# Kernel optimization log

Hardware: AMD Instinct MI355X
Metric: run time of the kernel (lower is better)

The kernel has to match this reference:

```python
import jax, jax.numpy as jnp
import numpy as np

N, E, D, H, G, O = 50000, 800000, 128, 256, 128, 10
BN_EPS = 1e-5
SLOPE = 0.2  # LeakyReLU negative slope


def setup_inputs() -> dict:
    keys = iter(jax.random.split(jax.random.key(0), 64))

    def rn(shape, scale=0.05):
        return jax.random.normal(next(keys), shape, jnp.float32) * scale

    inp = {
        "x": jax.random.normal(next(keys), (N, D), jnp.float32),
        "edge_index": jax.random.randint(next(keys), (2, E), 0, N),
        "edge_attr": jax.random.normal(next(keys), (E, 3), jnp.float32),
        "batch": jnp.sort(jax.random.randint(next(keys), (N,), 0, G)),
    }
    for i, din in zip((1, 2, 3), (D, H, H)):
        inp[f"We{i}"] = rn((3, din))
        inp[f"be{i}"] = jnp.zeros((din,), jnp.float32)
        inp[f"W{i}1"] = rn((din, H))
        inp[f"b{i}1"] = jnp.zeros((H,), jnp.float32)
        inp[f"g{i}"] = jnp.ones((H,), jnp.float32)
        inp[f"bt{i}"] = jnp.zeros((H,), jnp.float32)
        inp[f"mu{i}"] = jnp.zeros((H,), jnp.float32)
        inp[f"var{i}"] = jnp.ones((H,), jnp.float32)
        inp[f"W{i}2"] = rn((H, H))
        inp[f"b{i}2"] = jnp.zeros((H,), jnp.float32)
    for name, shape in (("Wm1", (3 * H, 200)), ("Wm2", (200, 200)), ("Wm3", (200, 200)), ("Wm4", (200, O))):
        inp[name] = rn(shape)
        inp["b" + name[1:]] = jnp.zeros((shape[1],), jnp.float32)
    return inp


def _leaky(v):
    return jax.nn.leaky_relu(v, SLOPE)


def _gine(x, src, dst, ea, We, be, W1, b1, g, bt, mu, var, W2, b2):
    # message: ReLU(x_j + lin_edge(edge_attr)); aggregate: scatter-sum to dst
    msg = jax.nn.relu(x[src] + ea @ We + be)          # [E, din]
    agg = jax.ops.segment_sum(msg, dst, num_segments=N)  # [N, din]
    h = x + agg                                       # (1+eps)*x_i + agg, eps=0
    h = h @ W1 + b1
    h = g * (h - mu) * jax.lax.rsqrt(var + BN_EPS) + bt  # BatchNorm1d (eval)
    h = _leaky(h)
    return _leaky(h @ W2 + b2)


def reference(x, edge_index, edge_attr, batch,
              We1, be1, W11, b11, g1, bt1, mu1, var1, W12, b12,
              We2, be2, W21, b21, g2, bt2, mu2, var2, W22, b22,
              We3, be3, W31, b31, g3, bt3, mu3, var3, W32, b32,
              Wm1, bm1, Wm2, bm2, Wm3, bm3, Wm4, bm4):
    src, dst = edge_index[0], edge_index[1]
    x1 = _gine(x, src, dst, edge_attr, We1, be1, W11, b11, g1, bt1, mu1, var1, W12, b12)
    x2 = _gine(x1, src, dst, edge_attr, We2, be2, W21, b21, g2, bt2, mu2, var2, W22, b22)
    x3 = _gine(x2, src, dst, edge_attr, We3, be3, W31, b31, g3, bt3, mu3, var3, W32, b32)
    p1 = jax.ops.segment_sum(x1, batch, num_segments=G)  # global_add_pool
    p2 = jax.ops.segment_sum(x2, batch, num_segments=G)
    p3 = jax.ops.segment_sum(x3, batch, num_segments=G)
    h = jnp.concatenate((p1, p2, p3), axis=1)            # [G, 3H]
    # MLP (dropout is identity at inference); note doubled LeakyReLU in source
    h = _leaky(_leaky(h @ Wm1 + bm1))
    h = _leaky(_leaky(h @ Wm2 + bm2))
    h = _leaky(_leaky(h @ Wm3 + bm3))
    return h @ Wm4 + bm4                                 # [G, O]
```

## Files before the change

### kernel.cpp

```cpp
#include <hip/hip_runtime.h>
#include <hip/hip_fp16.h>

#define LRELU(v) ((v) >= 0.f ? (v) : 0.2f * (v))
#define DLRELU(v) ((v) >= 0.f ? (v) : 0.04f * (v))

constexpr int Nn = 50000;
constexpr int Ee = 800000;
constexpr int Hh = 256;
constexpr int Gg = 128;
constexpr int Oo = 10;

typedef __attribute__((ext_vector_type(8))) short short8;
typedef __attribute__((ext_vector_type(4))) float f32x4;
typedef __attribute__((ext_vector_type(4))) unsigned int uv4;
typedef __attribute__((ext_vector_type(2))) unsigned int uv2;
typedef __attribute__((ext_vector_type(4))) unsigned short us4;

__device__ inline unsigned short f2h(float f) {
  __half h = __float2half_rn(f);
  return *reinterpret_cast<unsigned short*>(&h);
}
__device__ inline float h2f(unsigned short u) {
  __half h = *reinterpret_cast<__half*>(&u);
  return __half2float(h);
}
__device__ inline __half2 u2h2(unsigned int u) {
  return *reinterpret_cast<__half2*>(&u);
}
__device__ inline unsigned int h22u(__half2 h) {
  return *reinterpret_cast<unsigned int*>(&h);
}
__device__ inline __half2 hmax2(__half2 a, __half2 b) {
  __half2 r;
  asm volatile("v_pk_max_f16 %0, %1, %2" : "=v"(r) : "v"(a), "v"(b));
  return r;
}
__device__ inline unsigned short f2bf(float f) {
  union { float f; unsigned int i; } v; v.f = f;
  unsigned int i = v.i;
  return (unsigned short)((i + 0x7FFFu + ((i >> 16) & 1u)) >> 16);
}

typedef __attribute__((address_space(1))) const unsigned int gu32;
typedef __attribute__((address_space(3))) unsigned int lu32;
__device__ inline void gload_lds16(const void* g, void* l) {
  __builtin_amdgcn_global_load_lds((gu32*)g, (lu32*)l, 16, 0, 0);
}

__global__ __launch_bounds__(256) void hist_kernel(
    const int* __restrict__ dst, int* __restrict__ deg)
{
  const int e = blockIdx.x * 256 + threadIdx.x;
  if (e < Ee) atomicAdd(&deg[dst[e]], 1);
}

__global__ __launch_bounds__(1024) void scan1_kernel(
    const int* __restrict__ deg, int* __restrict__ bsum)
{
  const int i = blockIdx.x * 1024 + threadIdx.x;
  int v = (i < Nn) ? deg[i] : 0;
  #pragma unroll
  for (int o = 32; o; o >>= 1) v += __shfl_xor(v, o, 64);
  __shared__ int ws[16];
  const int wid = threadIdx.x >> 6, lane = threadIdx.x & 63;
  if (lane == 0) ws[wid] = v;
  __syncthreads();
  if (threadIdx.x == 0) {
    int s = 0;
    #pragma unroll
    for (int k = 0; k < 16; k++) s += ws[k];
    bsum[blockIdx.x] = s;
  }
}

__global__ __launch_bounds__(64) void scan2_kernel(
    const int* __restrict__ bsum, int* __restrict__ boff, int* __restrict__ row_ptr, int nb)
{
  if (threadIdx.x == 0) {
    int s = 0;
    for (int b = 0; b < nb; b++) { boff[b] = s; s += bsum[b]; }
    row_ptr[Nn] = s;
  }
}

__global__ __launch_bounds__(1024) void scan3_kernel(
    const int* __restrict__ deg, const int* __restrict__ boff,
    int* __restrict__ row_ptr, int* __restrict__ cursor)
{
  const int i = blockIdx.x * 1024 + threadIdx.x;
  const int wid = threadIdx.x >> 6, lane = threadIdx.x & 63;
  const int v = (i < Nn) ? deg[i] : 0;
  int inc = v;
  #pragma unroll
  for (int o = 1; o < 64; o <<= 1) {
    const int u = __shfl_up(inc, o, 64);
    if (lane >= o) inc += u;
  }
  __shared__ int ws[16];
  if (lane == 63) ws[wid] = inc;
  __syncthreads();
  if (wid == 0 && lane < 16) {
    int s = ws[lane];
    #pragma unroll
    for (int o = 1; o < 16; o <<= 1) {
      const int u = __shfl_up(s, o, 64);
      if (lane >= o) s += u;
    }
    ws[lane] = s;
  }
  __syncthreads();
  const int woff = (wid == 0) ? 0 : ws[wid - 1];
  const int excl = boff[blockIdx.x] + woff + inc - v;
  if (i < Nn) { row_ptr[i] = excl; cursor[i] = excl; }
}

__global__ __launch_bounds__(256) void fill_kernel(
    const int* __restrict__ src, const int* __restrict__ dst,
    const float* __restrict__ ea, int* __restrict__ cursor,
    uv4* __restrict__ edges)
{
  const int e = blockIdx.x * 256 + threadIdx.x;
  if (e >= Ee) return;
  const int pos = atomicAdd(&cursor[dst[e]], 1);
  uv4 r;
  r.x = (unsigned)src[e];
  r.y = h22u(__float2half2_rn(ea[3 * e + 0]));
  r.z = h22u(__float2half2_rn(ea[3 * e + 1]));
  r.w = h22u(__float2half2_rn(ea[3 * e + 2]));
  edges[pos] = r;
}

__global__ __launch_bounds__(256) void f2h_kernel(
    const float* __restrict__ in, unsigned short* __restrict__ out, int n4)
{
  const int i = blockIdx.x * 256 + threadIdx.x;
  if (i >= n4) return;
  const float4 v = *reinterpret_cast<const float4*>(in + (size_t)i * 4);
  us4 o; o.x = f2h(v.x); o.y = f2h(v.y); o.z = f2h(v.z); o.w = f2h(v.w);
  *reinterpret_cast<us4*>(out + (size_t)i * 4) = o;
}

struct WtJobs {
  const float* src[10];
  unsigned short* dst[10];
  int K[10], M[10], Kpad[10], isbf[10], blk0[11];
};

__global__ __launch_bounds__(256) void wtall_kernel(WtJobs J)
{
  int j = 0;
  #pragma unroll
  for (int q = 1; q < 10; q++) if ((int)blockIdx.x >= J.blk0[q]) j = q;
  const int g = ((int)blockIdx.x - J.blk0[j]) * 256 + threadIdx.x;
  const int Kpad = J.Kpad[j];
  if (g >= 256 * Kpad) return;
  const int c = g / Kpad, k = g % Kpad;
  const int K = J.K[j], M = J.M[j];
  unsigned short o = 0;
  if (c < M && k < K) {
    const float w = J.src[j][(size_t)k * M + c];
    o = J.isbf[j] ? f2bf(w) : f2h(w);
  }
  J.dst[j][(size_t)c * Kpad + k] = o;
}

template<int DIN>
__global__ __launch_bounds__(256) void agg_gather(
    const unsigned short* __restrict__ x, const uv4* __restrict__ edges,
    const float* __restrict__ We, const float* __restrict__ be,
    const int* __restrict__ row_ptr, unsigned short* __restrict__ S)
{
  constexpr int FPL = DIN / 64;
  constexpr int H2  = FPL / 2;
  constexpr int SH  = (DIN == 256) ? 8 : 7;
  const int wv   = threadIdx.x >> 6;
  const int lane = threadIdx.x & 63;
  const int n = blockIdx.x * 4 + wv;
  if (n >= Nn) return;
  const int fo = lane * FPL;

  const __half2 zero2 = __float2half2_rn(0.f);
  __half2 w0h[H2], w1h[H2], w2h[H2], bbh[H2], acc[H2];
  #pragma unroll
  for (int j = 0; j < H2; j++) {
    w0h[j] = __halves2half2(__float2half_rn(We[0 * DIN + fo + 2 * j]),
                            __float2half_rn(We[0 * DIN + fo + 2 * j + 1]));
    w1h[j] = __halves2half2(__float2half_rn(We[1 * DIN + fo + 2 * j]),
                            __float2half_rn(We[1 * DIN + fo + 2 * j + 1]));
    w2h[j] = __halves2half2(__float2half_rn(We[2 * DIN + fo + 2 * j]),
                            __float2half_rn(We[2 * DIN + fo + 2 * j + 1]));
    bbh[j] = __halves2half2(__float2half_rn(be[fo + 2 * j]),
                            __float2half_rn(be[fo + 2 * j + 1]));
    acc[j] = zero2;
  }

  const int beg = row_ptr[n], end = row_ptr[n + 1];
  int i = beg;

  for (; i + 8 <= end; i += 8) {
    uv4 e[8];
    #pragma unroll
    for (int q = 0; q < 8; q++) e[q] = __builtin_nontemporal_load(edges + i + q);
    __half2 xv[8][H2];
    #pragma unroll
    for (int q = 0; q < 8; q++) {
      const unsigned o = (e[q].x << SH) + fo;
      if constexpr (H2 == 2) {
        const uv2 r = *reinterpret_cast<const uv2*>(x + o);
        xv[q][0] = u2h2(r.x); xv[q][1] = u2h2(r.y);
      } else {
        xv[q][0] = u2h2(*reinterpret_cast<const unsigned int*>(x + o));
      }
    }
    #pragma unroll
    for (int q = 0; q < 8; q++) {
      const __half2 a0 = u2h2(e[q].y), a1 = u2h2(e[q].z), a2 = u2h2(e[q].w);
      #pragma unroll
      for (int j = 0; j < H2; j++) {
        __half2 m = __hadd2(xv[q][j], bbh[j]);
        m = __hfma2(a2, w2h[j], m);
        m = __hfma2(a1, w1h[j], m);
        m = __hfma2(a0, w0h[j], m);
        acc[j] = __hadd2(acc[j], hmax2(m, zero2));
      }
    }
  }
  for (; i < end; i++) {
    const uv4 e0 = __builtin_nontemporal_load(edges + i);
    const unsigned o0 = (e0.x << SH) + fo;
    __half2 xv0[H2];
    if constexpr (H2 == 2) {
      const uv2 r0 = *reinterpret_cast<const uv2*>(x + o0);
      xv0[0] = u2h2(r0.x); xv0[1] = u2h2(r0.y);
    } else {
      xv0[0] = u2h2(*reinterpret_cast<const unsigned int*>(x + o0));
    }
    const __half2 a00 = u2h2(e0.y), a01 = u2h2(e0.z), a02 = u2h2(e0.w);
    #pragma unroll
    for (int j = 0; j < H2; j++) {
      __half2 m0 = __hadd2(xv0[j], bbh[j]);
      m0 = __hfma2(a02, w2h[j], m0);
      m0 = __hfma2(a01, w1h[j], m0);
      m0 = __hfma2(a00, w0h[j], m0);
      acc[j] = __hadd2(acc[j], hmax2(m0, zero2));
    }
  }

  const unsigned on = ((unsigned)n << SH) + fo;
  if constexpr (H2 == 2) {
    const uv2 rs = *reinterpret_cast<const uv2*>(x + on);
    const float2 s0 = __half22float2(u2h2(rs.x)), s1 = __half22float2(u2h2(rs.y));
    const float2 f0 = __half22float2(acc[0]), f1 = __half22float2(acc[1]);
    uv2 o;
    o.x = (unsigned)f2h(s0.x + f0.x) | ((unsigned)f2h(s0.y + f0.y) << 16);
    o.y = (unsigned)f2h(s1.x + f1.x) | ((unsigned)f2h(s1.y + f1.y) << 16);
    __builtin_nontemporal_store(o, reinterpret_cast<uv2*>(S + on));
  } else {
    const float2 s0 = __half22float2(u2h2(*reinterpret_cast<const unsigned int*>(x + on)));
    const float2 f0 = __half22float2(acc[0]);
    const unsigned o = (unsigned)f2h(s0.x + f0.x) | ((unsigned)f2h(s0.y + f0.y) << 16);
    __builtin_nontemporal_store(o, reinterpret_cast<unsigned int*>(S + on));
  }
}

template<int K1, bool WRITE_XB>
__global__ __launch_bounds__(512) void gemm12(
    const unsigned short* __restrict__ A,
    const unsigned short* __restrict__ B1t, const float* __restrict__ b1,
    const float* __restrict__ gamma, const float* __restrict__ beta,
    const float* __restrict__ mu, const float* __restrict__ var,
    const unsigned short* __restrict__ B2t, const float* __restrict__ b2,
    unsigned short* __restrict__ XB,
    const int* __restrict__ batch, float* __restrict__ pooled, int layer)
{
  __shared__ __align__(16) unsigned short smem[128 * 256];
  unsigned short* lA = smem;
  unsigned short* lY = smem;
  float* part = (float*)smem;

  const int t = threadIdx.x;
  const int lane = t & 63, wid = t >> 6;
  const int wrow = wid >> 2, wcol = wid & 3;
  const int l15 = lane & 15, hi = lane >> 4;
  const int n0 = blockIdx.x * 128;

  constexpr int SPR = K1 / 8;
  constexpr int NCH = 128 * K1 * 2 / 1024;
  constexpr int CPW = NCH / 8;
  #pragma unroll
  for (int c = 0; c < CPW; c++) {
    const int ch = wid * CPW + c;
    const int row = ch * (512 / K1) + lane / SPR;
    const int slot = lane % SPR;
    const int scol = (slot ^ (row & 7)) * 8;
    const int gr = min(n0 + row, Nn - 1);
    gload_lds16(A + (size_t)gr * K1 + scol, (char*)lA + ch * 1024);
  }
  __syncthreads();

  f32x4 acc[4][4] = {};
  #pragma unroll
  for (int ks = 0; ks < K1 / 32; ks++) {
    short8 av[4], bv[4];
    #pragma unroll
    for (int rf = 0; rf < 4; rf++) {
      const int ar = wrow * 64 + rf * 16 + l15;
      av[rf] = *reinterpret_cast<const short8*>(
          (const char*)lA + ar * (K1 * 2) + (((ks * 4 + hi) ^ (ar & 7)) << 4));
    }
    #pragma unroll
    for (int cf = 0; cf < 4; cf++) {
      const int c = wcol * 64 + cf * 16 + l15;
      bv[cf] = *reinterpret_cast<const short8*>(B1t + (size_t)c * K1 + ks * 32 + hi * 8);
    }
    #pragma unroll
    for (int rf = 0; rf < 4; rf++)
      #pragma unroll
      for (int cf = 0; cf < 4; cf++)
        acc[rf][cf] = __builtin_amdgcn_mfma_f32_16x16x32_f16(av[rf], bv[cf], acc[rf][cf], 0, 0, 0);
  }
  __syncthreads();

  #pragma unroll
  for (int cf = 0; cf < 4; cf++) {
    const int c = wcol * 64 + cf * 16 + l15;
    const float bs = b1[c];
    const float gm = gamma[c], bt2 = beta[c], mm = mu[c];
    const float iv = rsqrtf(var[c] + 1e-5f);
    const int slot0 = c >> 3;
    #pragma unroll
    for (int rf = 0; rf < 4; rf++)
      #pragma unroll
      for (int rg = 0; rg < 4; rg++) {
        const int row = wrow * 64 + rf * 16 + hi * 4 + rg;
        float v = acc[rf][cf][rg] + bs;
        v = gm * (v - mm) * iv + bt2;
        v = LRELU(v);
        *reinterpret_cast<unsigned short*>(
            (char*)lY + row * 512 + (((slot0 ^ (row & 7)) << 4)) + (c & 7) * 2) = f2h(v);
      }
  }
  __syncthreads();

  #pragma unroll
  for (int rf = 0; rf < 4; rf++)
    #pragma unroll
    for (int cf = 0; cf < 4; cf++) acc[rf][cf] = (f32x4){0.f, 0.f, 0.f, 0.f};
  #pragma unroll
  for (int ks = 0; ks < 8; ks++) {
    short8 av[4], bv[4];
    #pragma unroll
    for (int rf = 0; rf < 4; rf++) {
      const int ar = wrow * 64 + rf * 16 + l15;
      av[rf] = *reinterpret_cast<const short8*>(
          (const char*)lY + ar * 512 + (((ks * 4 + hi) ^ (ar & 7)) << 4));
    }
    #pragma unroll
    for (int cf = 0; cf < 4; cf++) {
      const int c = wcol * 64 + cf * 16 + l15;
      bv[cf] = *reinterpret_cast<const short8*>(B2t + (size_t)c * 256 + ks * 32 + hi * 8);
    }
    #pragma unroll
    for (int rf = 0; rf < 4; rf++)
      #pragma unroll
      for (int cf = 0; cf < 4; cf++)
        acc[rf][cf] = __builtin_amdgcn_mfma_f32_16x16x32_f16(av[rf], bv[cf], acc[rf][cf], 0, 0, 0);
  }
  __syncthreads();

  for (int z = t; z < 1024; z += 512) part[z] = 0.f;
  __syncthreads();

  const int base = batch[min(n0, Nn - 1)];
  int slotArr[4][4];
  #pragma unroll
  for (int rf = 0; rf < 4; rf++)
    #pragma unroll
    for (int rg = 0; rg < 4; rg++) {
      const int row = n0 + wrow * 64 + rf * 16 + hi * 4 + rg;
      slotArr[rf][rg] = (row < Nn) ? (batch[row] - base) : -1;
    }

  #pragma unroll
  for (int cf = 0; cf < 4; cf++) {
    const int col = wcol * 64 + cf * 16 + l15;
    const float bs = b2[col];
    float psum[4] = {0.f, 0.f, 0.f, 0.f};
    #pragma unroll
    for (int rf = 0; rf < 4; rf++)
      #pragma unroll
      for (int rg = 0; rg < 4; rg++) {
        const int sl = slotArr[rf][rg];
        if (sl < 0) continue;
        const float v = LRELU(acc[rf][cf][rg] + bs);
        if (WRITE_XB) {
          const int row = n0 + wrow * 64 + rf * 16 + hi * 4 + rg;
          XB[(size_t)row * 256 + col] = f2h(v);
        }
        psum[sl] += v;
      }
    #pragma unroll
    for (int k = 0; k < 4; k++)
      if (psum[k] != 0.f) atomicAdd(&part[k * 256 + col], psum[k]);
  }
  __syncthreads();

  for (int z = t; z < 1024; z += 512) {
    const float v = part[z];
    if (v != 0.f) {
      const int g = base + (z >> 8);
      if (g < Gg)
        atomicAdd(&pooled[(size_t)g * 768 + layer * 256 + (z & 255)], v);
    }
  }
}

__global__ __launch_bounds__(256) void head_fused(
    const float* __restrict__ P,
    const unsigned short* __restrict__ B1t,
    const unsigned short* __restrict__ B2t,
    const unsigned short* __restrict__ B3t,
    const unsigned short* __restrict__ B4t,
    const float* __restrict__ b1, const float* __restrict__ b2,
    const float* __restrict__ b3, const float* __restrict__ b4,
    float* __restrict__ out)
{
  __shared__ __align__(16) unsigned short act[32 * 256];
  const int t = threadIdx.x, lane = t & 63, wid = t >> 6;
  const int l15 = lane & 15, hi = lane >> 4;
  const int r0 = blockIdx.x * 32;

  f32x4 acc[2][4];

  #pragma unroll
  for (int rf = 0; rf < 2; rf++)
    #pragma unroll
    for (int cf = 0; cf < 4; cf++) acc[rf][cf] = (f32x4){0.f, 0.f, 0.f, 0.f};
  for (int ks = 0; ks < 24; ks++) {
    short8 bv[4], av[2];
    #pragma unroll
    for (int cf = 0; cf < 4; cf++) {
      const int c = wid * 64 + cf * 16 + l15;
      bv[cf] = *reinterpret_cast<const short8*>(B1t + (size_t)c * 768 + ks * 32 + hi * 8);
    }
    #pragma unroll
    for (int rf = 0; rf < 2; rf++) {
      const float* p = P + (size_t)(r0 + rf * 16 + l15) * 768 + ks * 32 + hi * 8;
      const float4 p0 = *reinterpret_cast<const float4*>(p);
      const float4 p1 = *reinterpret_cast<const float4*>(p + 4);
      short8 a;
      a[0] = (short)f2bf(p0.x); a[1] = (short)f2bf(p0.y);
      a[2] = (short)f2bf(p0.z); a[3] = (short)f2bf(p0.w);
      a[4] = (short)f2bf(p1.x); a[5] = (short)f2bf(p1.y);
      a[6] = (short)f2bf(p1.z); a[7] = (short)f2bf(p1.w);
      av[rf] = a;
    }
    #pragma unroll
    for (int rf = 0; rf < 2; rf++)
      #pragma unroll
      for (int cf = 0; cf < 4; cf++)
        acc[rf][cf] = __builtin_amdgcn_mfma_f32_16x16x32_bf16(av[rf], bv[cf], acc[rf][cf], 0, 0, 0);
  }
  #pragma unroll
  for (int cf = 0; cf < 4; cf++) {
    const int c = wid * 64 + cf * 16 + l15;
    const float bs = (c < 200) ? b1[c] : 0.f;
    const int slot0 = c >> 3;
    #pragma unroll
    for (int rf = 0; rf < 2; rf++)
      #pragma unroll
      for (int rg = 0; rg < 4; rg++) {
        const int row = rf * 16 + hi * 4 + rg;
        const float v = DLRELU(acc[rf][cf][rg] + bs);
        act[row * 256 + ((slot0 ^ (row & 7)) << 3) + (c & 7)] = f2bf(v);
      }
  }
  __syncthreads();

  #pragma unroll
  for (int L = 0; L < 2; L++) {
    const unsigned short* B = (L == 0) ? B2t : B3t;
    const float* bias = (L == 0) ? b2 : b3;
    #pragma unroll
    for (int rf = 0; rf < 2; rf++)
      #pragma unroll
      for (int cf = 0; cf < 4; cf++) acc[rf][cf] = (f32x4){0.f, 0.f, 0.f, 0.f};
    #pragma unroll
    for (int ks = 0; ks < 8; ks++) {
      short8 bv[4], av[2];
      #pragma unroll
      for (int cf = 0; cf < 4; cf++) {
        const int c = wid * 64 + cf * 16 + l15;
        bv[cf] = *reinterpret_cast<const short8*>(B + (size_t)c * 256 + ks * 32 + hi * 8);
      }
      #pragma unroll
      for (int rf = 0; rf < 2; rf++) {
        const int row = rf * 16 + l15;
        const int slot = ks * 4 + hi;
        av[rf] = *reinterpret_cast<const short8*>(
            act + row * 256 + ((slot ^ (row & 7)) << 3));
      }
      #pragma unroll
      for (int rf = 0; rf < 2; rf++)
        #pragma unroll
        for (int cf = 0; cf < 4; cf++)
          acc[rf][cf] = __builtin_amdgcn_mfma_f32_16x16x32_bf16(av[rf], bv[cf], acc[rf][cf], 0, 0, 0);
    }
    __syncthreads();
    #pragma unroll
    for (int cf = 0; cf < 4; cf++) {
      const int c = wid * 64 + cf * 16 + l15;
      const float bs = (c < 200) ? bias[c] : 0.f;
      const int slot0 = c >> 3;
      #pragma unroll
      for (int rf = 0; rf < 2; rf++)
        #pragma unroll
        for (int rg = 0; rg < 4; rg++) {
          const int row = rf * 16 + hi * 4 + rg;
          const float v = DLRELU(acc[rf][cf][rg] + bs);
          act[row * 256 + ((slot0 ^ (row & 7)) << 3) + (c & 7)] = f2bf(v);
        }
    }
    __syncthreads();
  }

  if (wid == 0) {
    f32x4 a4[2] = {};
    #pragma unroll
    for (int ks = 0; ks < 8; ks++) {
      short8 av[2];
      const short8 bv = *reinterpret_cast<const short8*>(
          B4t + (size_t)l15 * 256 + ks * 32 + hi * 8);
      #pragma unroll
      for (int rf = 0; rf < 2; rf++) {
        const int row = rf * 16 + l15;
        const int slot = ks * 4 + hi;
        av[rf] = *reinterpret_cast<const short8*>(
            act + row * 256 + ((slot ^ (row & 7)) << 3));
      }
      #pragma unroll
      for (int rf = 0; rf < 2; rf++)
        a4[rf] = __builtin_amdgcn_mfma_f32_16x16x32_bf16(av[rf], bv, a4[rf], 0, 0, 0);
    }
    if (l15 < Oo) {
      const float bs = b4[l15];
      #pragma unroll
      for (int rf = 0; rf < 2; rf++)
        #pragma unroll
        for (int rg = 0; rg < 4; rg++) {
          const int row = r0 + rf * 16 + hi * 4 + rg;
          out[(size_t)row * Oo + l15] = a4[rf][rg] + bs;
        }
    }
  }
}

extern "C" void kernel_launch(void* const* d_in, const int* in_sizes, int n_in,
                              void* d_out, int out_size, void* d_ws, size_t ws_size,
                              hipStream_t stream)
{
  const float* x     = (const float*)d_in[0];
  const int*   ei    = (const int*)d_in[1];
  const float* ea    = (const float*)d_in[2];
  const int*   batch = (const int*)d_in[3];
  const int* src = ei;
  const int* dst = ei + Ee;

  const float *We[3], *be_[3], *W1[3], *b1[3], *g_[3], *bt_[3], *mu_[3], *var_[3], *W2[3], *b2[3];
  for (int l = 0; l < 3; l++) {
    const int base = 4 + l * 10;
    We[l]  = (const float*)d_in[base + 0];
    be_[l] = (const float*)d_in[base + 1];
    W1[l]  = (const float*)d_in[base + 2];
    b1[l]  = (const float*)d_in[base + 3];
    g_[l]  = (const float*)d_in[base + 4];
    bt_[l] = (const float*)d_in[base + 5];
    mu_[l] = (const float*)d_in[base + 6];
    var_[l]= (const float*)d_in[base + 7];
    W2[l]  = (const float*)d_in[base + 8];
    b2[l]  = (const float*)d_in[base + 9];
  }
  const float *Wm[4], *bm[4];
  for (int i = 0; i < 4; i++) {
    Wm[i] = (const float*)d_in[34 + 2 * i];
    bm[i] = (const float*)d_in[35 + 2 * i];
  }

  int* deg     = (int*)d_ws;
  int* cursor  = deg + Nn;
  int* row_ptr = cursor + Nn;
  int* bsum    = row_ptr + Nn + 4;
  int* boff    = bsum + 64;
  uv4* edges   = (uv4*)(boff + 64);
  unsigned short* x0h  = (unsigned short*)(edges + Ee);
  unsigned short* Wt11 = x0h + (size_t)Nn * 128;
  unsigned short* Wt12 = Wt11 + 32768;
  unsigned short* Wt21 = Wt12 + 65536;
  unsigned short* Wt22 = Wt21 + 65536;
  unsigned short* Wt31 = Wt22 + 65536;
  unsigned short* Wt32 = Wt31 + 65536;
  unsigned short* HW1t = Wt32 + 65536;
  unsigned short* HW2t = HW1t + 256 * 768;
  unsigned short* HW3t = HW2t + 65536;
  unsigned short* HW4t = HW3t + 65536;
  unsigned short* S    = HW4t + 65536;
  unsigned short* XB0  = S  + (size_t)Nn * Hh;
  unsigned short* XB1  = XB0 + (size_t)Nn * Hh;
  float* pooled = (float*)(XB1 + (size_t)Nn * Hh);
  float* outf  = (float*)d_out;

  const int  gemmGrid = (Nn + 127) / 128;
  const int  aggGrid  = (Nn + 3) / 4;
  const int  eGrid    = (Ee + 255) / 256;
  const int  sGrid    = (Nn + 1023) / 1024;

  hipMemsetAsync(deg, 0, Nn * sizeof(int), stream);
  hipMemsetAsync(pooled, 0, (size_t)Gg * 768 * sizeof(float), stream);

  hist_kernel<<<eGrid, 256, 0, stream>>>(dst, deg);
  scan1_kernel<<<sGrid, 1024, 0, stream>>>(deg, bsum);
  scan2_kernel<<<1, 64, 0, stream>>>(bsum, boff, row_ptr, sGrid);
  scan3_kernel<<<sGrid, 1024, 0, stream>>>(deg, boff, row_ptr, cursor);
  fill_kernel<<<eGrid, 256, 0, stream>>>(src, dst, ea, cursor, edges);

  f2h_kernel<<<(Nn * 128 / 4 + 255) / 256, 256, 0, stream>>>(x, x0h, Nn * 128 / 4);
  {
    WtJobs J;
    const float* s[10] = {W1[0], W2[0], W1[1], W2[1], W1[2], W2[2], Wm[0], Wm[1], Wm[2], Wm[3]};
    unsigned short* d[10] = {Wt11, Wt12, Wt21, Wt22, Wt31, Wt32, HW1t, HW2t, HW3t, HW4t};
    const int Ks[10]   = {128, 256, 256, 256, 256, 256, 768, 200, 200, 200};
    const int Ms[10]   = {256, 256, 256, 256, 256, 256, 200, 200, 200, 10};
    const int Kp[10]   = {128, 256, 256, 256, 256, 256, 768, 256, 256, 256};
    const int bf[10]   = {0, 0, 0, 0, 0, 0, 1, 1, 1, 1};
    int blk = 0;
    for (int q = 0; q < 10; q++) {
      J.src[q] = s[q]; J.dst[q] = d[q];
      J.K[q] = Ks[q]; J.M[q] = Ms[q]; J.Kpad[q] = Kp[q]; J.isbf[q] = bf[q];
      J.blk0[q] = blk;
      blk += (256 * Kp[q] + 255) / 256;
    }
    J.blk0[10] = blk;
    wtall_kernel<<<blk, 256, 0, stream>>>(J);
  }

  agg_gather<128><<<aggGrid, 256, 0, stream>>>(x0h, edges, We[0], be_[0], row_ptr, S);
  gemm12<128, true><<<gemmGrid, 512, 0, stream>>>(
      S, Wt11, b1[0], g_[0], bt_[0], mu_[0], var_[0], Wt12, b2[0], XB0,
      batch, pooled, 0);

  agg_gather<256><<<aggGrid, 256, 0, stream>>>(XB0, edges, We[1], be_[1], row_ptr, S);
  gemm12<256, true><<<gemmGrid, 512, 0, stream>>>(
      S, Wt21, b1[1], g_[1], bt_[1], mu_[1], var_[1], Wt22, b2[1], XB1,
      batch, pooled, 1);

  agg_gather<256><<<aggGrid, 256, 0, stream>>>(XB1, edges, We[2], be_[2], row_ptr, S);
  gemm12<256, false><<<gemmGrid, 512, 0, stream>>>(
      S, Wt31, b1[2], g_[2], bt_[2], mu_[2], var_[2], Wt32, b2[2], nullptr,
      batch, pooled, 2);

  head_fused<<<4, 256, 0, stream>>>(pooled, HW1t, HW2t, HW3t, HW4t,
                                    bm[0], bm[1], bm[2], bm[3], outf);
}
```

Measured before the change: 552.7 us.

## Merge prep kernels into one launch, shrink gather unroll, hoist batch-slot loads

Folds the fp32-to-fp16 input conversion, the degree histogram and the weight transpose/convert jobs into a single prep kernel dispatched by block range, removing two kernel launches and letting the pieces run concurrently. The edge-gather main loop unroll drops from 8 to 4 edges per iteration, which should lower register pressure at the cost of fewer loads in flight. The batch-slot lookups in the GEMM epilogue are moved earlier, ahead of the first epilogue, so their latency can overlap other work, at the cost of keeping those registers live longer.

```diff
diff --git a/kernel.cpp b/kernel.cpp
--- a/kernel.cpp
+++ b/kernel.cpp
@@ -47,11 +47,45 @@
   __builtin_amdgcn_global_load_lds((gu32*)g, (lu32*)l, 16, 0, 0);
 }
 
-__global__ __launch_bounds__(256) void hist_kernel(
-    const int* __restrict__ dst, int* __restrict__ deg)
-{
-  const int e = blockIdx.x * 256 + threadIdx.x;
-  if (e < Ee) atomicAdd(&deg[dst[e]], 1);
+struct PrepArgs {
+  const float* x; unsigned short* x0h;
+  const int* dst; int* deg;
+  const float* wsrc[10];
+  unsigned short* wdst[10];
+  int K[10], M[10], Kpad[10], isbf[10], blk0[11];
+};
+constexpr int PREP_A = (Nn * 128 / 4 + 255) / 256;
+constexpr int PREP_B = (Ee + 255) / 256;
+
+__global__ __launch_bounds__(256) void prep_kernel(PrepArgs P)
+{
+  const int bid = blockIdx.x;
+  if (bid < PREP_A) {
+    const int i = bid * 256 + threadIdx.x;
+    if (i >= Nn * 128 / 4) return;
+    const float4 v = *reinterpret_cast<const float4*>(P.x + (size_t)i * 4);
+    us4 o; o.x = f2h(v.x); o.y = f2h(v.y); o.z = f2h(v.z); o.w = f2h(v.w);
+    *reinterpret_cast<us4*>(P.x0h + (size_t)i * 4) = o;
+    return;
+  }
+  if (bid < PREP_A + PREP_B) {
+    const int e = (bid - PREP_A) * 256 + threadIdx.x;
+    if (e < Ee) atomicAdd(&P.deg[P.dst[e]], 1);
+    return;
+  }
+  int j = 0;
+  #pragma unroll
+  for (int q = 1; q < 10; q++) if (bid >= P.blk0[q]) j = q;
+  const int g = (bid - P.blk0[j]) * 256 + threadIdx.x;
+  const int Kpad = P.Kpad[j];
+  if (g >= 256 * Kpad) return;
+  const int c = g / Kpad, k = g % Kpad;
+  unsigned short o = 0;
+  if (c < P.M[j] && k < P.K[j]) {
+    const float w = P.wsrc[j][(size_t)k * P.M[j] + c];
+    o = P.isbf[j] ? f2bf(w) : f2h(w);
+  }
+  P.wdst[j][(size_t)c * Kpad + k] = o;
 }
 
 __global__ __launch_bounds__(1024) void scan1_kernel(
@@ -128,40 +162,6 @@
   r.z = h22u(__float2half2_rn(ea[3 * e + 1]));
   r.w = h22u(__float2half2_rn(ea[3 * e + 2]));
   edges[pos] = r;
-}
-
-__global__ __launch_bounds__(256) void f2h_kernel(
-    const float* __restrict__ in, unsigned short* __restrict__ out, int n4)
-{
-  const int i = blockIdx.x * 256 + threadIdx.x;
-  if (i >= n4) return;
-  const float4 v = *reinterpret_cast<const float4*>(in + (size_t)i * 4);
-  us4 o; o.x = f2h(v.x); o.y = f2h(v.y); o.z = f2h(v.z); o.w = f2h(v.w);
-  *reinterpret_cast<us4*>(out + (size_t)i * 4) = o;
-}
-
-struct WtJobs {
-  const float* src[10];
-  unsigned short* dst[10];
-  int K[10], M[10], Kpad[10], isbf[10], blk0[11];
-};
-
-__global__ __launch_bounds__(256) void wtall_kernel(WtJobs J)
-{
-  int j = 0;
-  #pragma unroll
-  for (int q = 1; q < 10; q++) if ((int)blockIdx.x >= J.blk0[q]) j = q;
-  const int g = ((int)blockIdx.x - J.blk0[j]) * 256 + threadIdx.x;
-  const int Kpad = J.Kpad[j];
-  if (g >= 256 * Kpad) return;
-  const int c = g / Kpad, k = g % Kpad;
-  const int K = J.K[j], M = J.M[j];
-  unsigned short o = 0;
-  if (c < M && k < K) {
-    const float w = J.src[j][(size_t)k * M + c];
-    o = J.isbf[j] ? f2bf(w) : f2h(w);
-  }
-  J.dst[j][(size_t)c * Kpad + k] = o;
 }
 
 template<int DIN>
@@ -197,13 +197,13 @@
   const int beg = row_ptr[n], end = row_ptr[n + 1];
   int i = beg;
 
-  for (; i + 8 <= end; i += 8) {
-    uv4 e[8];
-    #pragma unroll
-    for (int q = 0; q < 8; q++) e[q] = __builtin_nontemporal_load(edges + i + q);
-    __half2 xv[8][H2];
-    #pragma unroll
-    for (int q = 0; q < 8; q++) {
+  for (; i + 4 <= end; i += 4) {
+    uv4 e[4];
+    #pragma unroll
+    for (int q = 0; q < 4; q++) e[q] = __builtin_nontemporal_load(edges + i + q);
+    __half2 xv[4][H2];
+    #pragma unroll
+    for (int q = 0; q < 4; q++) {
       const unsigned o = (e[q].x << SH) + fo;
       if constexpr (H2 == 2) {
         const uv2 r = *reinterpret_cast<const uv2*>(x + o);
@@ -213,7 +213,7 @@
       }
     }
     #pragma unroll
-    for (int q = 0; q < 8; q++) {
+    for (int q = 0; q < 4; q++) {
       const __half2 a0 = u2h2(e[q].y), a1 = u2h2(e[q].z), a2 = u2h2(e[q].w);
       #pragma unroll
       for (int j = 0; j < H2; j++) {
@@ -342,6 +342,16 @@
   }
   __syncthreads();
 
+  const int base = batch[min(n0, Nn - 1)];
+  int slotArr[4][4];
+  #pragma unroll
+  for (int rf = 0; rf < 4; rf++)
+    #pragma unroll
+    for (int rg = 0; rg < 4; rg++) {
+      const int row = n0 + wrow * 64 + rf * 16 + hi * 4 + rg;
+      slotArr[rf][rg] = (row < Nn) ? (batch[row] - base) : -1;
+    }
+
   #pragma unroll
   for (int rf = 0; rf < 4; rf++)
     #pragma unroll
@@ -370,16 +380,6 @@
 
   for (int z = t; z < 1024; z += 512) part[z] = 0.f;
   __syncthreads();
-
-  const int base = batch[min(n0, Nn - 1)];
-  int slotArr[4][4];
-  #pragma unroll
-  for (int rf = 0; rf < 4; rf++)
-    #pragma unroll
-    for (int rg = 0; rg < 4; rg++) {
-      const int row = n0 + wrow * 64 + rf * 16 + hi * 4 + rg;
-      slotArr[rf][rg] = (row < Nn) ? (batch[row] - base) : -1;
-    }
 
   #pragma unroll
   for (int cf = 0; cf < 4; cf++) {
@@ -617,32 +617,31 @@
   hipMemsetAsync(deg, 0, Nn * sizeof(int), stream);
   hipMemsetAsync(pooled, 0, (size_t)Gg * 768 * sizeof(float), stream);
 
-  hist_kernel<<<eGrid, 256, 0, stream>>>(dst, deg);
+  {
+    PrepArgs P;
+    P.x = x; P.x0h = x0h; P.dst = dst; P.deg = deg;
+    const float* s[10] = {W1[0], W2[0], W1[1], W2[1], W1[2], W2[2], Wm[0], Wm[1], Wm[2], Wm[3]};
+    unsigned short* d[10] = {Wt11, Wt12, Wt21, Wt22, Wt31, Wt32, HW1t, HW2t, HW3t, HW4t};
+    const int Ks[10] = {128, 256, 256, 256, 256, 256, 768, 200, 200, 200};
+    const int Ms[10] = {256, 256, 256, 256, 256, 256, 200, 200, 200, 10};
+    const int Kp[10] = {128, 256, 256, 256, 256, 256, 768, 256, 256, 256};
+    const int bf[10] = {0, 0, 0, 0, 0, 0, 1, 1, 1, 1};
+    int blk = PREP_A + PREP_B;
+    for (int q = 0; q < 10; q++) {
+      P.wsrc[q] = s[q]; P.wdst[q] = d[q];
+      P.K[q] = Ks[q]; P.M[q] = Ms[q]; P.Kpad[q] = Kp[q]; P.isbf[q] = bf[q];
+      P.blk0[q] = blk;
+      blk += Kp[q];
+    }
+    P.blk0[10] = blk;
+    prep_kernel<<<blk, 256, 0, stream>>>(P);
+  }
+
   scan1_kernel<<<sGrid, 1024, 0, stream>>>(deg, bsum);
   scan2_kernel<<<1, 64, 0, stream>>>(bsum, boff, row_ptr, sGrid);
   scan3_kernel<<<sGrid, 1024, 0, stream>>>(deg, boff, row_ptr, cursor);
   fill_kernel<<<eGrid, 256, 0, stream>>>(src, dst, ea, cursor, edges);
 
-  f2h_kernel<<<(Nn * 128 / 4 + 255) / 256, 256, 0, stream>>>(x, x0h, Nn * 128 / 4);
-  {
-    WtJobs J;
-    const float* s[10] = {W1[0], W2[0], W1[1], W2[1], W1[2], W2[2], Wm[0], Wm[1], Wm[2], Wm[3]};
-    unsigned short* d[10] = {Wt11, Wt12, Wt21, Wt22, Wt31, Wt32, HW1t, HW2t, HW3t, HW4t};
-    const int Ks[10]   = {128, 256, 256, 256, 256, 256, 768, 200, 200, 200};
-    const int Ms[10]   = {256, 256, 256, 256, 256, 256, 200, 200, 200, 10};
-    const int Kp[10]   = {128, 256, 256, 256, 256, 256, 768, 256, 256, 256};
-    const int bf[10]   = {0, 0, 0, 0, 0, 0, 1, 1, 1, 1};
-    int blk = 0;
-    for (int q = 0; q < 10; q++) {
-      J.src[q] = s[q]; J.dst[q] = d[q];
-      J.K[q] = Ks[q]; J.M[q] = Ms[q]; J.Kpad[q] = Kp[q]; J.isbf[q] = bf[q];
-      J.blk0[q] = blk;
-      blk += (256 * Kp[q] + 255) / 256;
-    }
-    J.blk0[10] = blk;
-    wtall_kernel<<<blk, 256, 0, stream>>>(J);
-  }
-
   agg_gather<128><<<aggGrid, 256, 0, stream>>>(x0h, edges, We[0], be_[0], row_ptr, S);
   gemm12<128, true><<<gemmGrid, 512, 0, stream>>>(
       S, Wt11, b1[0], g_[0], bt_[0], mu_[0], var_[0], Wt12, b2[0], XB0,
```

After: 537.2 us. 1.03x faster.
